# Kernel tuning notes

Measured on AMD Instinct MI355X. Metric: run time of the kernel, lower is better.

The kernel has to match this reference:

```python
import jax, jax.numpy as jnp
import numpy as np

BATCH = 50000      # number of target nodes in the batch (len(to_neighs))
DEGREE = 32        # fixed sampled neighbor count per node
NUM_NODES = 500000 # embedding table size (id2feat domain)
D_FEAT = 128       # feature dim of id2feat


def setup_inputs() -> dict:
    key = jax.random.key(0)
    k1, k2 = jax.random.split(key)
    neighs = jax.random.randint(k1, (BATCH, DEGREE), 0, NUM_NODES, dtype=jnp.int64)
    id2feat_table = jax.random.normal(k2, (NUM_NODES, D_FEAT), dtype=jnp.float32) * 0.02
    return {"neighs": neighs, "id2feat_table": id2feat_table}


def reference(neighs, id2feat_table):
    # Original: mask counts each neighbor occurrence, row-normalized by num_neigh,
    # then mask @ embed_matrix == per-node mean of neighbor embeddings.
    # Fixed degree K, so segment-mean == gather + mean over the neighbor axis.
    neigh_feats = id2feat_table[neighs]        # [B, K, D] gather (memory-bound)
    to_feats = neigh_feats.mean(axis=1)        # [B, D] mean over K neighbors
    return to_feats
```

## Files before the change

kernel.cpp:

```cpp
#include <hip/hip_runtime.h>
#include <hip/hip_bf16.h>


constexpr int BATCH  = 50000;
constexpr int DEGREE = 32;
constexpr int D_FEAT = 128;

__global__ __launch_bounds__(256) void MeanAggregator_841813590039_kernel(
    const int* __restrict__ neighs,
    const float* __restrict__ table,
    float* __restrict__ out)
{
    const int gtid = blockIdx.x * blockDim.x + threadIdx.x;
    const int node = gtid >> 6;
    const int lane = threadIdx.x & 63;
    if (node >= BATCH) return;

    const int* __restrict__ idx = neighs + node * DEGREE;

    float2 acc = make_float2(0.f, 0.f);

    #pragma unroll
    for (int k = 0; k < DEGREE; ++k) {
        const int row = idx[k];
        const float2* __restrict__ p =
            reinterpret_cast<const float2*>(table + (size_t)row * D_FEAT);
        const float2 v = p[lane];
        acc.x += v.x;
        acc.y += v.y;
    }

    const float inv = 1.0f / (float)DEGREE;
    float2* __restrict__ o =
        reinterpret_cast<float2*>(out + (size_t)node * D_FEAT);
    o[lane] = make_float2(acc.x * inv, acc.y * inv);
}

extern "C" void kernel_launch(void* const* d_in, const int* in_sizes, int n_in,
                              void* d_out, int out_size, void* d_ws, size_t ws_size,
                              hipStream_t stream) {
    const int*   neighs = (const int*)d_in[0];
    const float* table  = (const float*)d_in[1];
    float*       out    = (float*)d_out;

    const int waves_per_block = 256 / 64;
    const int grid = (BATCH + waves_per_block - 1) / waves_per_block;

    MeanAggregator_841813590039_kernel<<<grid, 256, 0, stream>>>(neighs, table, out);
}
```

Measured before the change: 405.8 us.

## Convert table to fp16 in workspace and gather half-precision rows

Result: no change. 399.5 us (-1.5%).

```diff
diff --git a/kernel.cpp b/kernel.cpp
--- a/kernel.cpp
+++ b/kernel.cpp
@@ -1,38 +1,95 @@
 #include <hip/hip_runtime.h>
 #include <hip/hip_bf16.h>
+#include <hip/hip_fp16.h>
 
 
-constexpr int BATCH  = 50000;
-constexpr int DEGREE = 32;
-constexpr int D_FEAT = 128;
+constexpr int BATCH     = 50000;
+constexpr int DEGREE    = 32;
+constexpr int D_FEAT    = 128;
+constexpr int NUM_NODES = 500000;
 
-__global__ __launch_bounds__(256) void MeanAggregator_841813590039_kernel(
-    const int* __restrict__ neighs,
-    const float* __restrict__ table,
+typedef float        f32x4 __attribute__((ext_vector_type(4)));
+typedef unsigned int u32x4 __attribute__((ext_vector_type(4)));
+
+__global__ __launch_bounds__(256) void cvt_table_kernel(
+    const float* __restrict__ src, unsigned short* __restrict__ dst)
+{
+    const size_t base = ((size_t)blockIdx.x * 256 + threadIdx.x) * 8;
+    const f32x4* sp = reinterpret_cast<const f32x4*>(src + base);
+    f32x4 a = __builtin_nontemporal_load(sp);
+    f32x4 b = __builtin_nontemporal_load(sp + 1);
+
+    float v[8] = {a.x, a.y, a.z, a.w, b.x, b.y, b.z, b.w};
+    unsigned int h[8];
+#pragma unroll
+    for (int j = 0; j < 8; ++j) {
+        __half hh = __float2half(v[j]);
+        h[j] = (unsigned int)__half_as_ushort(hh);
+    }
+    u32x4 o;
+    o.x = h[0] | (h[1] << 16);
+    o.y = h[2] | (h[3] << 16);
+    o.z = h[4] | (h[5] << 16);
+    o.w = h[6] | (h[7] << 16);
+    *reinterpret_cast<u32x4*>(dst + base) = o;
+}
+
+__global__ __launch_bounds__(256) void gather_f16_kernel(
+    const int* __restrict__ neighs, const unsigned short* __restrict__ tab,
     float* __restrict__ out)
 {
-    const int gtid = blockIdx.x * blockDim.x + threadIdx.x;
-    const int node = gtid >> 6;
+    const int node = blockIdx.x * 4 + (threadIdx.x >> 6);
     const int lane = threadIdx.x & 63;
-    if (node >= BATCH) return;
 
     const int* __restrict__ idx = neighs + node * DEGREE;
 
+    int rows[DEGREE];
+#pragma unroll
+    for (int k = 0; k < DEGREE; ++k) rows[k] = idx[k];
+
+    unsigned int v[DEGREE];
+#pragma unroll
+    for (int k = 0; k < DEGREE; ++k) {
+        const unsigned int* p = reinterpret_cast<const unsigned int*>(
+            tab + (size_t)rows[k] * D_FEAT);
+        v[k] = p[lane];
+    }
+
     float2 acc = make_float2(0.f, 0.f);
-
-    #pragma unroll
+#pragma unroll
     for (int k = 0; k < DEGREE; ++k) {
-        const int row = idx[k];
-        const float2* __restrict__ p =
-            reinterpret_cast<const float2*>(table + (size_t)row * D_FEAT);
-        const float2 v = p[lane];
-        acc.x += v.x;
-        acc.y += v.y;
+        __half2 h = *reinterpret_cast<__half2*>(&v[k]);
+        float2 f = __half22float2(h);
+        acc.x += f.x;
+        acc.y += f.y;
     }
 
     const float inv = 1.0f / (float)DEGREE;
-    float2* __restrict__ o =
-        reinterpret_cast<float2*>(out + (size_t)node * D_FEAT);
+    typedef float f32x2 __attribute__((ext_vector_type(2)));
+    f32x2 r; r.x = acc.x * inv; r.y = acc.y * inv;
+    f32x2* o = reinterpret_cast<f32x2*>(out + (size_t)node * D_FEAT) + lane;
+    __builtin_nontemporal_store(r, o);
+}
+
+__global__ __launch_bounds__(256) void gather_f32_kernel(
+    const int* __restrict__ neighs, const float* __restrict__ table,
+    float* __restrict__ out)
+{
+    const int node = blockIdx.x * 4 + (threadIdx.x >> 6);
+    const int lane = threadIdx.x & 63;
+    const int* __restrict__ idx = neighs + node * DEGREE;
+
+    float2 acc = make_float2(0.f, 0.f);
+#pragma unroll
+    for (int k = 0; k < DEGREE; ++k) {
+        const float2* p = reinterpret_cast<const float2*>(
+            table + (size_t)idx[k] * D_FEAT);
+        float2 t = p[lane];
+        acc.x += t.x;
+        acc.y += t.y;
+    }
+    const float inv = 1.0f / (float)DEGREE;
+    float2* o = reinterpret_cast<float2*>(out + (size_t)node * D_FEAT);
     o[lane] = make_float2(acc.x * inv, acc.y * inv);
 }
 
@@ -43,8 +100,14 @@
     const float* table  = (const float*)d_in[1];
     float*       out    = (float*)d_out;
 
-    const int waves_per_block = 256 / 64;
-    const int grid = (BATCH + waves_per_block - 1) / waves_per_block;
+    const size_t ws_needed = (size_t)NUM_NODES * D_FEAT * sizeof(unsigned short);
 
-    MeanAggregator_841813590039_kernel<<<grid, 256, 0, stream>>>(neighs, table, out);
+    if (ws_size >= ws_needed) {
+        unsigned short* tab16 = (unsigned short*)d_ws;
+        const int cvt_grid = (NUM_NODES * D_FEAT / 8 + 255) / 256;
+        cvt_table_kernel<<<cvt_grid, 256, 0, stream>>>(table, tab16);
+        gather_f16_kernel<<<BATCH / 4, 256, 0, stream>>>(neighs, tab16, out);
+    } else {
+        gather_f32_kernel<<<BATCH / 4, 256, 0, stream>>>(neighs, table, out);
+    }
 }
```

## Split gather into two table-range passes to improve L2/MALL locality

Applied to the files above, without the earlier changes.

Result: slower. 433.5 us (+6.9%).

```diff
diff --git a/kernel.cpp b/kernel.cpp
--- a/kernel.cpp
+++ b/kernel.cpp
@@ -1,39 +1,63 @@
 #include <hip/hip_runtime.h>
-#include <hip/hip_bf16.h>
 
 
-constexpr int BATCH  = 50000;
-constexpr int DEGREE = 32;
-constexpr int D_FEAT = 128;
+constexpr int BATCH     = 50000;
+constexpr int DEGREE    = 32;
+constexpr int D_FEAT    = 128;
+constexpr int NUM_NODES = 500000;
+constexpr int SPLIT     = NUM_NODES / 2;
 
-__global__ __launch_bounds__(256) void MeanAggregator_841813590039_kernel(
+typedef float f32x2 __attribute__((ext_vector_type(2)));
+
+__global__ __launch_bounds__(256) void gather_window_kernel(
     const int* __restrict__ neighs,
     const float* __restrict__ table,
-    float* __restrict__ out)
+    float* __restrict__ out,
+    int lo, int hi, int final_pass)
 {
-    const int gtid = blockIdx.x * blockDim.x + threadIdx.x;
-    const int node = gtid >> 6;
+    int node = blockIdx.x * 4 + (threadIdx.x >> 6);
+    node = __builtin_amdgcn_readfirstlane(node);
     const int lane = threadIdx.x & 63;
-    if (node >= BATCH) return;
 
-    const int* __restrict__ idx = neighs + node * DEGREE;
+    const int* __restrict__ idx = neighs + (size_t)node * DEGREE;
+
+    int rows[DEGREE];
+#pragma unroll
+    for (int k = 0; k < DEGREE; ++k) rows[k] = idx[k];
+
+    int   r[DEGREE];
+    float w[DEGREE];
+#pragma unroll
+    for (int k = 0; k < DEGREE; ++k) {
+        const bool in = (rows[k] >= lo) && (rows[k] < hi);
+        r[k] = in ? rows[k] : 0;
+        w[k] = in ? 1.0f : 0.0f;
+    }
+
+    float2 v[DEGREE];
+#pragma unroll
+    for (int k = 0; k < DEGREE; ++k)
+        v[k] = reinterpret_cast<const float2*>(table + (size_t)r[k] * D_FEAT)[lane];
 
     float2 acc = make_float2(0.f, 0.f);
-
-    #pragma unroll
+#pragma unroll
     for (int k = 0; k < DEGREE; ++k) {
-        const int row = idx[k];
-        const float2* __restrict__ p =
-            reinterpret_cast<const float2*>(table + (size_t)row * D_FEAT);
-        const float2 v = p[lane];
-        acc.x += v.x;
-        acc.y += v.y;
+        acc.x = fmaf(w[k], v[k].x, acc.x);
+        acc.y = fmaf(w[k], v[k].y, acc.y);
     }
 
-    const float inv = 1.0f / (float)DEGREE;
-    float2* __restrict__ o =
-        reinterpret_cast<float2*>(out + (size_t)node * D_FEAT);
-    o[lane] = make_float2(acc.x * inv, acc.y * inv);
+    f32x2* o = reinterpret_cast<f32x2*>(out + (size_t)node * D_FEAT) + lane;
+    if (final_pass) {
+        f32x2 prev = *o;
+        f32x2 res;
+        const float inv = 1.0f / (float)DEGREE;
+        res.x = (acc.x + prev.x) * inv;
+        res.y = (acc.y + prev.y) * inv;
+        __builtin_nontemporal_store(res, o);
+    } else {
+        f32x2 p; p.x = acc.x; p.y = acc.y;
+        *o = p;
+    }
 }
 
 extern "C" void kernel_launch(void* const* d_in, const int* in_sizes, int n_in,
@@ -43,8 +67,9 @@
     const float* table  = (const float*)d_in[1];
     float*       out    = (float*)d_out;
 
-    const int waves_per_block = 256 / 64;
-    const int grid = (BATCH + waves_per_block - 1) / waves_per_block;
-
-    MeanAggregator_841813590039_kernel<<<grid, 256, 0, stream>>>(neighs, table, out);
+    const int grid = BATCH / 4;
+    gather_window_kernel<<<grid, 256, 0, stream>>>(neighs, table, out,
+                                                   0, SPLIT, 0);
+    gather_window_kernel<<<grid, 256, 0, stream>>>(neighs, table, out,
+                                                   SPLIT, NUM_NODES, 1);
 }
```

## Process two nodes per wave with float4 loads and shuffled indices

Applied to the files above, without the earlier changes.

Measured after the change: 399.2 us. Within noise of the previous version (-1.6%).

```diff
diff --git a/kernel.cpp b/kernel.cpp
--- a/kernel.cpp
+++ b/kernel.cpp
@@ -1,39 +1,57 @@
 #include <hip/hip_runtime.h>
-#include <hip/hip_bf16.h>
 
 
 constexpr int BATCH  = 50000;
 constexpr int DEGREE = 32;
 constexpr int D_FEAT = 128;
 
+typedef float f32x4 __attribute__((ext_vector_type(4)));
+
 __global__ __launch_bounds__(256) void MeanAggregator_841813590039_kernel(
     const int* __restrict__ neighs,
     const float* __restrict__ table,
     float* __restrict__ out)
 {
-    const int gtid = blockIdx.x * blockDim.x + threadIdx.x;
-    const int node = gtid >> 6;
-    const int lane = threadIdx.x & 63;
-    if (node >= BATCH) return;
+    const int wave  = (blockIdx.x * 256 + threadIdx.x) >> 6;
+    const int lane  = threadIdx.x & 63;
+    const int nodeA = wave * 2;
+    const int col   = lane & 31;
+    const int half  = lane & 32;
 
-    const int* __restrict__ idx = neighs + node * DEGREE;
+    const int rows = neighs[(size_t)nodeA * DEGREE + lane];
 
-    float2 acc = make_float2(0.f, 0.f);
+    #define ROW(k) __shfl(rows, half + (k), 64)
+    #define LOADK(k) \
+        reinterpret_cast<const f32x4*>(table + (size_t)ROW(k) * D_FEAT)[col]
+
+    f32x4 buf0[8], buf1[8];
 
     #pragma unroll
-    for (int k = 0; k < DEGREE; ++k) {
-        const int row = idx[k];
-        const float2* __restrict__ p =
-            reinterpret_cast<const float2*>(table + (size_t)row * D_FEAT);
-        const float2 v = p[lane];
-        acc.x += v.x;
-        acc.y += v.y;
+    for (int j = 0; j < 8; ++j) buf0[j] = LOADK(j);
+
+    f32x4 acc = {0.f, 0.f, 0.f, 0.f};
+
+    #pragma unroll
+    for (int g = 0; g < 3; ++g) {
+        f32x4* cur = (g & 1) ? buf1 : buf0;
+        f32x4* nxt = (g & 1) ? buf0 : buf1;
+        #pragma unroll
+        for (int j = 0; j < 8; ++j) nxt[j] = LOADK((g + 1) * 8 + j);
+        #pragma unroll
+        for (int j = 0; j < 8; ++j) acc += cur[j];
     }
+    #pragma unroll
+    for (int j = 0; j < 8; ++j) acc += buf1[j];
+
+    #undef LOADK
+    #undef ROW
 
     const float inv = 1.0f / (float)DEGREE;
-    float2* __restrict__ o =
-        reinterpret_cast<float2*>(out + (size_t)node * D_FEAT);
-    o[lane] = make_float2(acc.x * inv, acc.y * inv);
+    acc *= inv;
+
+    const int node = nodeA + (half >> 5);
+    f32x4* o = reinterpret_cast<f32x4*>(out + (size_t)node * D_FEAT) + col;
+    __builtin_nontemporal_store(acc, o);
 }
 
 extern "C" void kernel_launch(void* const* d_in, const int* in_sizes, int n_in,
@@ -43,8 +61,6 @@
     const float* table  = (const float*)d_in[1];
     float*       out    = (float*)d_out;
 
-    const int waves_per_block = 256 / 64;
-    const int grid = (BATCH + waves_per_block - 1) / waves_per_block;
-
+    const int grid = BATCH / 8;
     MeanAggregator_841813590039_kernel<<<grid, 256, 0, stream>>>(neighs, table, out);
 }
```
